# Kernel tuning notes

Measured on AMD Instinct MI355X. Metric: run time of the kernel, lower is better.

## Reference

```python
import jax, jax.numpy as jnp
import numpy as np

DEPTH = 18                      # perfect binary tree depth -> N = 2**DEPTH - 1 nodes
N_NODES = 2 ** DEPTH - 1        # 262143
VOCAB, E, H = 2048, 64, 64


def setup_inputs() -> dict:
    key = jax.random.key(0)
    ks = jax.random.split(key, 10)
    token_ids = jax.random.randint(ks[0], (N_NODES,), 0, VOCAB, dtype=jnp.int32)
    emb = jax.random.normal(ks[1], (VOCAB, E), dtype=jnp.float32)
    emb = emb.at[0].set(0.0)  # padding_idx=0 row is zero in torch
    s = 0.1  # keep gates out of hard saturation
    return {
        "token_ids": token_ids,
        "emb": emb,
        "W_iou": jax.random.normal(ks[2], (3 * H, E), dtype=jnp.float32) * s,
        "b_Wiou": jnp.zeros((3 * H,), dtype=jnp.float32),
        "U_iou": jax.random.normal(ks[3], (3 * H, 2 * H), dtype=jnp.float32) * s,
        "b_Uiou": jnp.zeros((3 * H,), dtype=jnp.float32),
        "W_f": jax.random.normal(ks[4], (2 * H, E), dtype=jnp.float32) * s,
        "b_Wf": jnp.zeros((2 * H,), dtype=jnp.float32),
        "U_f": jax.random.normal(ks[5], (2 * H, 2 * H), dtype=jnp.float32) * s,
        "b_Uf": jnp.zeros((2 * H,), dtype=jnp.float32),
        "depth": DEPTH,
    }


def _tree_lstm(token_ids, emb, W_iou, b_Wiou, U_iou, b_Uiou, W_f, b_Wf, U_f, b_Uf, depth):
    """Level-synchronous bottom-up Binary TreeLSTM over a perfect binary tree.

    Node i has children 2i+1 (left), 2i+2 (right); level l occupies
    indices [2**l - 1, 2**(l+1) - 2]. Children of level-l node k sit at
    offsets 2k, 2k+1 of level l+1, so a reshape gives (left, right) pairs.
    """
    Hd = W_f.shape[0] // 2
    h = c = None
    for l in range(depth - 1, -1, -1):
        start, n = 2 ** l - 1, 2 ** l
        x = emb[token_ids[start:start + n]]                    # [n, E]
        if h is None:  # leaves: zero left/right states (both children zero)
            h_cat = jnp.zeros((n, 2 * Hd), dtype=x.dtype)
            c_lr = jnp.zeros((n, 2, Hd), dtype=x.dtype)
        else:
            h_cat = h.reshape(n, 2 * Hd)                        # [h_l | h_r]
            c_lr = c.reshape(n, 2, Hd)
        iou = jax.nn.sigmoid(x @ W_iou.T + b_Wiou + h_cat @ U_iou.T + b_Uiou)
        i_g, o_g, u_g = jnp.split(iou, 3, axis=1)
        u_g = jnp.tanh(u_g)  # faithful: tanh(sigmoid(u_pre)) as in the source
        f = jax.nn.sigmoid(x @ W_f.T + b_Wf + h_cat @ U_f.T + b_Uf)
        f_l, f_r = f[:, :Hd], f[:, Hd:]
        c = i_g * u_g + f_l * c_lr[:, 0] + f_r * c_lr[:, 1]
        h = o_g * jnp.tanh(c)
    return jnp.stack([h, c])  # [2, 1, H]: root (h, c)


def reference(token_ids, emb, W_iou, b_Wiou, U_iou, b_Uiou, W_f, b_Wf, U_f, b_Uf, depth):
    return _tree_lstm(token_ids, emb, W_iou, b_Wiou, U_iou, b_Uiou,
                      W_f, b_Wf, U_f, b_Uf, depth)
```

## Files before the change

### kernel.cpp

```cpp
#include <hip/hip_runtime.h>

typedef __bf16 bf16;
typedef __bf16 bf16x8 __attribute__((ext_vector_type(8)));
typedef float f32x4 __attribute__((ext_vector_type(4)));

#define DEPTH   18
#define N_NODES ((1 << DEPTH) - 1)
#define KDIM    192
#define RDIM    320
#define A_PAD   200
#define LOG2E   1.4426950408889634f

__device__ __forceinline__ float rcpf(float x) { return __builtin_amdgcn_rcpf(x); }
__device__ __forceinline__ float sig2(float p)  { return rcpf(1.f + exp2f(-p)); }
__device__ __forceinline__ float tanhf_(float x){ return 2.f * rcpf(1.f + exp2f(-2.f * LOG2E * x)) - 1.f; }

__device__ __forceinline__ void gates(const f32x4* acc,
        const float4& bI, const float4& bO, const float4& bU,
        const float4& bL, const float4& bR,
        const float4& cl, const float4& cr, float4& c4, float4& h4) {
    const float* pbI = &bI.x; const float* pbO = &bO.x; const float* pbU = &bU.x;
    const float* pbL = &bL.x; const float* pbR = &bR.x;
    const float* pcl = &cl.x; const float* pcr = &cr.x;
    float* pc4 = &c4.x; float* ph4 = &h4.x;
#pragma unroll
    for (int r = 0; r < 4; r++) {
        float i_g = sig2(acc[0][r] + pbI[r]);
        float o_g = sig2(acc[1][r] + pbO[r]);
        float u_g = tanhf_(sig2(acc[2][r] + pbU[r]));
        float fl  = sig2(acc[3][r] + pbL[r]);
        float fr  = sig2(acc[4][r] + pbR[r]);
        float c = i_g * u_g + fl * pcl[r] + fr * pcr[r];
        pc4[r] = c;
        ph4[r] = o_g * tanhf_(c);
    }
}

__global__ void prep_all(const float* __restrict__ emb,
                     const float* __restrict__ W_iou, const float* __restrict__ U_iou,
                     const float* __restrict__ W_f,   const float* __restrict__ U_f,
                     const float* __restrict__ b_Wiou, const float* __restrict__ b_Uiou,
                     const float* __restrict__ b_Wf,   const float* __restrict__ b_Uf,
                     bf16* __restrict__ Wcat, float* __restrict__ bias, bf16* __restrict__ emb16,
                     bf16* __restrict__ leafH, float* __restrict__ leafC) {
    __shared__ __align__(16) bf16 Wl[192 * 72];
    __shared__ __align__(16) bf16 Al[64 * 72];
    const int blk = blockIdx.x, tid = threadIdx.x;
    if (blk < 512) {
        int t = blk * 256 + tid;
        emb16[t] = (bf16)emb[t];
        if (t < RDIM * KDIM) {
            int r = t / KDIM, k = t % KDIM;
            float v;
            if (r < 192) v = (k < 64) ? W_iou[r * 64 + k] : U_iou[r * 128 + (k - 64)];
            else { int rr = r - 192; v = (k < 64) ? W_f[rr * 64 + k] : U_f[rr * 128 + (k - 64)]; }
            Wcat[t] = (bf16)(v * LOG2E);
        }
        if (t < RDIM)
            bias[t] = ((t < 192) ? (b_Wiou[t] + b_Uiou[t]) : (b_Wf[t - 192] + b_Uf[t - 192])) * LOG2E;
        return;
    }
    const int v0 = (blk - 512) * 64;
    for (int i = tid; i < 192 * 64; i += 256) {
        int r = i >> 6, k = i & 63;
        Wl[r * 72 + k] = (bf16)(W_iou[i] * LOG2E);
    }
    for (int i = tid; i < 64 * 64; i += 256) {
        int r = i >> 6, k = i & 63;
        Al[r * 72 + k] = (bf16)emb[(v0 << 6) + i];
    }
    __syncthreads();
    const int wave = tid >> 6, lane = tid & 63;
    const int l15 = lane & 15, quad = lane >> 4;
    const int jw = (wave & 3) * 16, jb = jw + quad * 4;

    f32x4 acc[4][3];
#pragma unroll
    for (int t = 0; t < 4; t++)
#pragma unroll
        for (int g = 0; g < 3; g++) acc[t][g] = (f32x4){0.f, 0.f, 0.f, 0.f};
#pragma unroll
    for (int kb = 0; kb < 2; kb++) {
        bf16x8 wfrag[3], nfrag[4];
#pragma unroll
        for (int g = 0; g < 3; g++)
            wfrag[g] = *(const bf16x8*)(&Wl[(g * 64 + jw + l15) * 72 + kb * 32 + quad * 8]);
#pragma unroll
        for (int t = 0; t < 4; t++)
            nfrag[t] = *(const bf16x8*)(&Al[(t * 16 + l15) * 72 + kb * 32 + quad * 8]);
#pragma unroll
        for (int t = 0; t < 4; t++)
#pragma unroll
            for (int g = 0; g < 3; g++)
                acc[t][g] = __builtin_amdgcn_mfma_f32_16x16x32_bf16(wfrag[g], nfrag[t], acc[t][g], 0, 0, 0);
    }
    float4 bW, bU_;
    bW = *(const float4*)(b_Wiou + jb);       bU_ = *(const float4*)(b_Uiou + jb);
    float4 bI = make_float4((bW.x + bU_.x) * LOG2E, (bW.y + bU_.y) * LOG2E, (bW.z + bU_.z) * LOG2E, (bW.w + bU_.w) * LOG2E);
    bW = *(const float4*)(b_Wiou + 64 + jb);  bU_ = *(const float4*)(b_Uiou + 64 + jb);
    float4 bO = make_float4((bW.x + bU_.x) * LOG2E, (bW.y + bU_.y) * LOG2E, (bW.z + bU_.z) * LOG2E, (bW.w + bU_.w) * LOG2E);
    bW = *(const float4*)(b_Wiou + 128 + jb); bU_ = *(const float4*)(b_Uiou + 128 + jb);
    float4 bU = make_float4((bW.x + bU_.x) * LOG2E, (bW.y + bU_.y) * LOG2E, (bW.z + bU_.z) * LOG2E, (bW.w + bU_.w) * LOG2E);
    const float* pbI = &bI.x; const float* pbO = &bO.x; const float* pbU = &bU.x;
#pragma unroll
    for (int t = 0; t < 4; t++) {
        int v = v0 + t * 16 + l15;
        float4 c4; float* pc4 = &c4.x;
        union { bf16 h[4]; uint2 u; } hp;
#pragma unroll
        for (int r = 0; r < 4; r++) {
            float i_g = sig2(acc[t][0][r] + pbI[r]);
            float o_g = sig2(acc[t][1][r] + pbO[r]);
            float u_g = tanhf_(sig2(acc[t][2][r] + pbU[r]));
            float c = i_g * u_g;
            pc4[r] = c;
            hp.h[r] = (bf16)(o_g * tanhf_(c));
        }
        *(float4*)(leafC + (size_t)v * 64 + jb) = c4;
        *(uint2*)(leafH + (size_t)v * 64 + jb) = hp.u;
    }
}

template<int NQ, bool CGLOB>
__device__ __forceinline__ void level_phase(
        int l, int blk, int tid, int wt, int l15, int quad, int jb,
        const bf16x8 (&Wf)[5][6],
        const float4& bI, const float4& bO, const float4& bU,
        const float4& bL, const float4& bR,
        bf16* Acur, bf16* Anx,
        const bf16* __restrict__ emb16, const int* __restrict__ token_ids,
        bf16* __restrict__ H, float* __restrict__ c_buf)
{
    const int m = 1 << (l - 8);
    const int s = (1 << l) - 1, o = blk * m;
    const int T = (m + 15) >> 4;
    const int mn = m >> 1;
    const float* Cin = (const float*)(Acur + m * A_PAD);

    float4 pcl[NQ], pcr[NQ];
    int pidx[NQ], pgn[NQ]; bool pact[NQ];
#pragma unroll
    for (int q = 0; q < NQ; q++) {
        int ti = wt + 2 * q;
        int idx0 = ti * 16 + l15;
        bool act = (ti < T) && (idx0 < m);
        int idx = act ? idx0 : 0;
        pidx[q] = idx; pact[q] = act; pgn[q] = s + o + idx;
        if (CGLOB) {
            pcl[q] = *(const float4*)(c_buf + (size_t)(2 * pgn[q] + 1) * 64 + jb);
            pcr[q] = *(const float4*)(c_buf + (size_t)(2 * pgn[q] + 2) * 64 + jb);
        } else {
            pcl[q] = *(const float4*)(Cin + (2 * idx) * 68 + jb);
            pcr[q] = *(const float4*)(Cin + (2 * idx + 1) * 68 + jb);
        }
    }

    int tok = 0;
    const int srow = tid >> 3, sk8 = (tid & 7) << 3;
    const bool sact = (l > 8) && (tid < mn * 8);
    if (sact) tok = token_ids[(1 << (l - 1)) - 1 + blk * mn + srow];

    float* Cout = (float*)(Anx + mn * A_PAD);
#pragma unroll
    for (int q = 0; q < NQ; q++) {
        f32x4 acc[5];
#pragma unroll
        for (int g = 0; g < 5; g++) acc[g] = (f32x4){0.f, 0.f, 0.f, 0.f};
#pragma unroll
        for (int kb = 0; kb < 6; kb++) {
            bf16x8 nf = *(const bf16x8*)(&Acur[pidx[q] * A_PAD + kb * 32 + quad * 8]);
#pragma unroll
            for (int g = 0; g < 5; g++)
                acc[g] = __builtin_amdgcn_mfma_f32_16x16x32_bf16(Wf[g][kb], nf, acc[g], 0, 0, 0);
        }
        float4 c4, h4;
        gates(acc, bI, bO, bU, bL, bR, pcl[q], pcr[q], c4, h4);
        if (pact[q]) {
            union { bf16 h[4]; uint2 u; } hp;
            const float* ph4 = &h4.x;
#pragma unroll
            for (int r = 0; r < 4; r++) hp.h[r] = (bf16)ph4[r];
            if (l > 8) {
                *(float4*)(Cout + pidx[q] * 68 + jb) = c4;
                *(uint2*)(&Anx[(pidx[q] >> 1) * A_PAD + 64 + (pidx[q] & 1) * 64 + jb]) = hp.u;
            } else {
                *(float4*)(c_buf + (size_t)pgn[q] * 64 + jb) = c4;
                *(uint2*)(H + (size_t)pgn[q] * 64 + jb) = hp.u;
            }
        }
    }

    if (sact) {
        uint4 g = *(const uint4*)(emb16 + (size_t)tok * 64 + sk8);
        *(uint4*)(&Anx[srow * A_PAD + sk8]) = g;
    }
    __syncthreads();
}

__global__ __launch_bounds__(512, 1) void big_pass(
        const bf16* __restrict__ Wcat, const float* __restrict__ bias,
        const bf16* __restrict__ emb16, const int* __restrict__ token_ids,
        const bf16* __restrict__ leafH, const float* __restrict__ leafC,
        bf16* __restrict__ H, float* __restrict__ c_buf) {
    __shared__ __align__(16) bf16 A0[256 * A_PAD];
    __shared__ __align__(16) bf16 A1[128 * A_PAD];
    const int tid = threadIdx.x, blk = blockIdx.x;
    const int wave = tid >> 6, lane = tid & 63;
    const int l15 = lane & 15, quad = lane >> 4;
    const int wj = wave & 3, wt = wave >> 2;
    const int jw = wj * 16, jb = jw + quad * 4;

    const int base16 = 65535 + blk * 256;

    for (int ch = tid; ch < 256 * 8; ch += 512) {
        int row = ch >> 3, k8 = (ch & 7) << 3;
        int tok = token_ids[base16 + row];
        *(uint4*)&A0[row * A_PAD + k8] = *(const uint4*)(emb16 + tok * 64 + k8);
    }
    for (int ch = tid; ch < 256 * 16; ch += 512) {
        int row = ch >> 4, half = (ch >> 3) & 1, k8 = (ch & 7) << 3;
        int tok = token_ids[2 * (base16 + row) + 1 + half];
        *(uint4*)&A0[row * A_PAD + 64 + half * 64 + k8] = *(const uint4*)(leafH + (size_t)tok * 64 + k8);
    }

    int tkl16[8], tkr16[8];
#pragma unroll
    for (int q = 0; q < 8; q++) {
        int idx = (wt + 2 * q) * 16 + l15;
        int gn = base16 + idx;
        tkl16[q] = token_ids[2 * gn + 1];
        tkr16[q] = token_ids[2 * gn + 2];
    }
    const int rowa = tid >> 3, k8a = (tid & 7) << 3;
    const int rowb = (tid + 512) >> 3, k8b = k8a;
    const int tok15a = token_ids[32767 + blk * 128 + rowa];
    const int tok15b = token_ids[32767 + blk * 128 + rowb];

    bf16x8 Wf[5][6];
#pragma unroll
    for (int g = 0; g < 5; g++)
#pragma unroll
        for (int kb = 0; kb < 6; kb++)
            Wf[g][kb] = *(const bf16x8*)(Wcat + (g * 64 + jw + l15) * KDIM + kb * 32 + quad * 8);

    const float4 bI = *(const float4*)(bias + jb);
    const float4 bO = *(const float4*)(bias + 64 + jb);
    const float4 bU = *(const float4*)(bias + 128 + jb);
    const float4 bL = *(const float4*)(bias + 192 + jb);
    const float4 bR = *(const float4*)(bias + 256 + jb);
    __syncthreads();

#pragma unroll
    for (int grp = 0; grp < 2; grp++) {
        float4 cl4[4], cr4[4];
#pragma unroll
        for (int q = 0; q < 4; q++) {
            cl4[q] = *(const float4*)(leafC + (size_t)tkl16[grp * 4 + q] * 64 + jb);
            cr4[q] = *(const float4*)(leafC + (size_t)tkr16[grp * 4 + q] * 64 + jb);
        }
#pragma unroll
        for (int q = 0; q < 4; q++) {
            const int idx = (wt + 2 * (grp * 4 + q)) * 16 + l15;
            const int gn = base16 + idx;
            f32x4 acc[5];
#pragma unroll
            for (int g = 0; g < 5; g++) acc[g] = (f32x4){0.f, 0.f, 0.f, 0.f};
#pragma unroll
            for (int kb = 0; kb < 6; kb++) {
                bf16x8 nf = *(const bf16x8*)(&A0[idx * A_PAD + kb * 32 + quad * 8]);
#pragma unroll
                for (int g = 0; g < 5; g++)
                    acc[g] = __builtin_amdgcn_mfma_f32_16x16x32_bf16(Wf[g][kb], nf, acc[g], 0, 0, 0);
            }
            float4 c4, h4;
            gates(acc, bI, bO, bU, bL, bR, cl4[q], cr4[q], c4, h4);
            union { bf16 h[4]; uint2 u; } hp;
            const float* ph4 = &h4.x;
#pragma unroll
            for (int r = 0; r < 4; r++) hp.h[r] = (bf16)ph4[r];
            *(float4*)(c_buf + (size_t)gn * 64 + jb) = c4;
            *(uint2*)(&A1[(idx >> 1) * A_PAD + 64 + (idx & 1) * 64 + jb]) = hp.u;
        }
        if (grp == 0) {
            uint4 ga = *(const uint4*)(emb16 + (size_t)tok15a * 64 + k8a);
            uint4 gb = *(const uint4*)(emb16 + (size_t)tok15b * 64 + k8b);
            *(uint4*)(&A1[rowa * A_PAD + k8a]) = ga;
            *(uint4*)(&A1[rowb * A_PAD + k8b]) = gb;
        }
    }
    __syncthreads();

    bf16* Acur = A1;
    bf16* Anx  = A0;
    level_phase<4, true >(15, blk, tid, wt, l15, quad, jb, Wf, bI, bO, bU, bL, bR,
                          Acur, Anx, emb16, token_ids, H, c_buf);
    { bf16* t = Acur; Acur = Anx; Anx = t; }
    level_phase<2, false>(14, blk, tid, wt, l15, quad, jb, Wf, bI, bO, bU, bL, bR,
                          Acur, Anx, emb16, token_ids, H, c_buf);
    { bf16* t = Acur; Acur = Anx; Anx = t; }
    for (int l = 13; l >= 8; l--) {
        level_phase<1, false>(l, blk, tid, wt, l15, quad, jb, Wf, bI, bO, bU, bL, bR,
                              Acur, Anx, emb16, token_ids, H, c_buf);
        bf16* t = Acur; Acur = Anx; Anx = t;
    }
}

__global__ __launch_bounds__(512) void tail_pass(
        const bf16* __restrict__ Wcat, const float* __restrict__ bias,
        const bf16* __restrict__ emb16, const int* __restrict__ token_ids,
        const bf16* __restrict__ H, const float* __restrict__ c_buf,
        float* __restrict__ out) {
    __shared__ __align__(16) bf16 A[255 * A_PAD];
    __shared__ __align__(16) float C0[128 * 68];
    __shared__ __align__(16) float C1[64 * 68];
    const int tid = threadIdx.x;
    const int wave = tid >> 6, lane = tid & 63;
    const int l15 = lane & 15, quad = lane >> 4;
    const int wj = wave & 3, wt = wave >> 2;
    const int jw = wj * 16, jb = jw + quad * 4;

    float4 cl7[4], cr7[4];
#pragma unroll
    for (int q = 0; q < 4; q++) {
        int idx = (wt + 2 * q) * 16 + l15;
        int gn = 127 + idx;
        cl7[q] = *(const float4*)(c_buf + (size_t)(2 * gn + 1) * 64 + jb);
        cr7[q] = *(const float4*)(c_buf + (size_t)(2 * gn + 2) * 64 + jb);
    }

    for (int ch = tid; ch < 255 * 8; ch += 512) {
        int row = ch >> 3, k8 = (ch & 7) << 3;
        int l = 31 - __clz(255 - row);
        int idx = row - 256 + (2 << l);
        int gn = (1 << l) - 1 + idx;
        int tok = token_ids[gn];
        *(uint4*)&A[row * A_PAD + k8] = *(const uint4*)(emb16 + tok * 64 + k8);
    }
    for (int ch = tid; ch < 128 * 16; ch += 512) {
        int row = ch >> 4, k8 = (ch & 15) << 3;
        *(uint4*)&A[row * A_PAD + 64 + k8] =
            *(const uint4*)(H + (size_t)(255 + 2 * row) * 64 + k8);
    }

    bf16x8 Wf[5][6];
#pragma unroll
    for (int g = 0; g < 5; g++)
#pragma unroll
        for (int kb = 0; kb < 6; kb++)
            Wf[g][kb] = *(const bf16x8*)(Wcat + (g * 64 + jw + l15) * KDIM + kb * 32 + quad * 8);

    const float4 bI = *(const float4*)(bias + jb);
    const float4 bO = *(const float4*)(bias + 64 + jb);
    const float4 bU = *(const float4*)(bias + 128 + jb);
    const float4 bL = *(const float4*)(bias + 192 + jb);
    const float4 bR = *(const float4*)(bias + 256 + jb);
    __syncthreads();

#pragma unroll
    for (int q = 0; q < 4; q++) {
        const int idx = (wt + 2 * q) * 16 + l15;
        f32x4 acc[5];
#pragma unroll
        for (int g = 0; g < 5; g++) acc[g] = (f32x4){0.f, 0.f, 0.f, 0.f};
#pragma unroll
        for (int kb = 0; kb < 6; kb++) {
            bf16x8 nf = *(const bf16x8*)(&A[idx * A_PAD + kb * 32 + quad * 8]);
#pragma unroll
            for (int g = 0; g < 5; g++)
                acc[g] = __builtin_amdgcn_mfma_f32_16x16x32_bf16(Wf[g][kb], nf, acc[g], 0, 0, 0);
        }
        float4 c4, h4;
        gates(acc, bI, bO, bU, bL, bR, cl7[q], cr7[q], c4, h4);
        union { bf16 h[4]; uint2 u; } hp;
        const float* ph4 = &h4.x;
#pragma unroll
        for (int r = 0; r < 4; r++) hp.h[r] = (bf16)ph4[r];
        *(float4*)(C0 + idx * 68 + jb) = c4;
        *(uint2*)(&A[(128 + (idx >> 1)) * A_PAD + 64 + (idx & 1) * 64 + jb]) = hp.u;
    }
    __syncthreads();

    float* Ccur = C0;
    float* Cnx  = C1;
    for (int l = 6; l >= 0; l--) {
        const int n = 1 << l;
        const int off  = 256 - 2 * n;
        const int offn = 256 - n;
        const int T = (n + 15) >> 4;
        for (int ti = wt; ti < T; ti += 2) {
            int idx0 = ti * 16 + l15;
            int idx = idx0 < n ? idx0 : n - 1;
            float4 cl = *(const float4*)(Ccur + (2 * idx) * 68 + jb);
            float4 cr = *(const float4*)(Ccur + (2 * idx + 1) * 68 + jb);
            f32x4 acc[5];
#pragma unroll
            for (int g = 0; g < 5; g++) acc[g] = (f32x4){0.f, 0.f, 0.f, 0.f};
#pragma unroll
            for (int kb = 0; kb < 6; kb++) {
                bf16x8 nf = *(const bf16x8*)(&A[(off + idx) * A_PAD + kb * 32 + quad * 8]);
#pragma unroll
                for (int g = 0; g < 5; g++)
                    acc[g] = __builtin_amdgcn_mfma_f32_16x16x32_bf16(Wf[g][kb], nf, acc[g], 0, 0, 0);
            }
            float4 c4, h4;
            gates(acc, bI, bO, bU, bL, bR, cl, cr, c4, h4);
            if (idx0 < n) {
                if (l > 0) {
                    union { bf16 h[4]; uint2 u; } hp;
                    const float* ph4 = &h4.x;
#pragma unroll
                    for (int r = 0; r < 4; r++) hp.h[r] = (bf16)ph4[r];
                    *(float4*)(Cnx + idx * 68 + jb) = c4;
                    *(uint2*)(&A[(offn + (idx >> 1)) * A_PAD + 64 + (idx & 1) * 64 + jb]) = hp.u;
                } else {
                    *(float4*)(out + jb) = h4;
                    *(float4*)(out + 64 + jb) = c4;
                }
            }
        }
        __syncthreads();
        float* t = Ccur; Ccur = Cnx; Cnx = t;
    }
}

extern "C" void kernel_launch(void* const* d_in, const int* in_sizes, int n_in,
                              void* d_out, int out_size, void* d_ws, size_t ws_size,
                              hipStream_t stream) {
    const int*   token_ids = (const int*)d_in[0];
    const float* emb       = (const float*)d_in[1];
    const float* W_iou     = (const float*)d_in[2];
    const float* b_Wiou    = (const float*)d_in[3];
    const float* U_iou     = (const float*)d_in[4];
    const float* b_Uiou    = (const float*)d_in[5];
    const float* W_f       = (const float*)d_in[6];
    const float* b_Wf      = (const float*)d_in[7];
    const float* U_f       = (const float*)d_in[8];
    const float* b_Uf      = (const float*)d_in[9];
    float* out = (float*)d_out;

    char* ws = (char*)d_ws;
    bf16*  Wcat  = (bf16*)ws;
    float* bias  = (float*)(ws + 122880);
    bf16*  emb16 = (bf16*)(ws + 124160);
    bf16*  leafH = (bf16*)(ws + 386304);
    float* leafC = (float*)(ws + 648448);
    bf16*  H     = (bf16*)(ws + 1172736);
    float* c_buf = (float*)(ws + 1238272);

    prep_all<<<544, 256, 0, stream>>>(emb, W_iou, U_iou, W_f, U_f,
                                      b_Wiou, b_Uiou, b_Wf, b_Uf,
                                      Wcat, bias, emb16, leafH, leafC);
    big_pass<<<256, 512, 0, stream>>>(Wcat, bias, emb16, token_ids, leafH, leafC, H, c_buf);
    tail_pass<<<1, 512, 0, stream>>>(Wcat, bias, emb16, token_ids, H, c_buf, out);
}
```

Baseline: 162.1 us.

## Fuse prep, big pass and tail into one cooperative kernel with grid syncs

Merges the three separate kernel launches (weight/embedding prep plus leaf computation, the per-block subtree pass, and the single-block tail) into one cooperative kernel. Grid-wide barriers replace the kernel boundaries. The leaf precompute is redistributed over the first 32 blocks of 512 threads, and shared memory is unified into one buffer reused by each phase. This removes launch gaps and kernel-boundary drains. In exchange it adds cooperative-launch overhead and grid-sync cost, and 255 blocks sit idle while block 0 runs the tail.

Result: slower. 236.0 us (+45.6%).

```diff
diff --git a/kernel.cpp b/kernel.cpp
--- a/kernel.cpp
+++ b/kernel.cpp
@@ -1,4 +1,7 @@
 #include <hip/hip_runtime.h>
+#include <hip/hip_cooperative_groups.h>
+
+namespace cg = cooperative_groups;
 
 typedef __bf16 bf16;
 typedef __bf16 bf16x8 __attribute__((ext_vector_type(8)));
@@ -33,91 +36,6 @@
         float c = i_g * u_g + fl * pcl[r] + fr * pcr[r];
         pc4[r] = c;
         ph4[r] = o_g * tanhf_(c);
-    }
-}
-
-__global__ void prep_all(const float* __restrict__ emb,
-                     const float* __restrict__ W_iou, const float* __restrict__ U_iou,
-                     const float* __restrict__ W_f,   const float* __restrict__ U_f,
-                     const float* __restrict__ b_Wiou, const float* __restrict__ b_Uiou,
-                     const float* __restrict__ b_Wf,   const float* __restrict__ b_Uf,
-                     bf16* __restrict__ Wcat, float* __restrict__ bias, bf16* __restrict__ emb16,
-                     bf16* __restrict__ leafH, float* __restrict__ leafC) {
-    __shared__ __align__(16) bf16 Wl[192 * 72];
-    __shared__ __align__(16) bf16 Al[64 * 72];
-    const int blk = blockIdx.x, tid = threadIdx.x;
-    if (blk < 512) {
-        int t = blk * 256 + tid;
-        emb16[t] = (bf16)emb[t];
-        if (t < RDIM * KDIM) {
-            int r = t / KDIM, k = t % KDIM;
-            float v;
-            if (r < 192) v = (k < 64) ? W_iou[r * 64 + k] : U_iou[r * 128 + (k - 64)];
-            else { int rr = r - 192; v = (k < 64) ? W_f[rr * 64 + k] : U_f[rr * 128 + (k - 64)]; }
-            Wcat[t] = (bf16)(v * LOG2E);
-        }
-        if (t < RDIM)
-            bias[t] = ((t < 192) ? (b_Wiou[t] + b_Uiou[t]) : (b_Wf[t - 192] + b_Uf[t - 192])) * LOG2E;
-        return;
-    }
-    const int v0 = (blk - 512) * 64;
-    for (int i = tid; i < 192 * 64; i += 256) {
-        int r = i >> 6, k = i & 63;
-        Wl[r * 72 + k] = (bf16)(W_iou[i] * LOG2E);
-    }
-    for (int i = tid; i < 64 * 64; i += 256) {
-        int r = i >> 6, k = i & 63;
-        Al[r * 72 + k] = (bf16)emb[(v0 << 6) + i];
-    }
-    __syncthreads();
-    const int wave = tid >> 6, lane = tid & 63;
-    const int l15 = lane & 15, quad = lane >> 4;
-    const int jw = (wave & 3) * 16, jb = jw + quad * 4;
-
-    f32x4 acc[4][3];
-#pragma unroll
-    for (int t = 0; t < 4; t++)
-#pragma unroll
-        for (int g = 0; g < 3; g++) acc[t][g] = (f32x4){0.f, 0.f, 0.f, 0.f};
-#pragma unroll
-    for (int kb = 0; kb < 2; kb++) {
-        bf16x8 wfrag[3], nfrag[4];
-#pragma unroll
-        for (int g = 0; g < 3; g++)
-            wfrag[g] = *(const bf16x8*)(&Wl[(g * 64 + jw + l15) * 72 + kb * 32 + quad * 8]);
-#pragma unroll
-        for (int t = 0; t < 4; t++)
-            nfrag[t] = *(const bf16x8*)(&Al[(t * 16 + l15) * 72 + kb * 32 + quad * 8]);
-#pragma unroll
-        for (int t = 0; t < 4; t++)
-#pragma unroll
-            for (int g = 0; g < 3; g++)
-                acc[t][g] = __builtin_amdgcn_mfma_f32_16x16x32_bf16(wfrag[g], nfrag[t], acc[t][g], 0, 0, 0);
-    }
-    float4 bW, bU_;
-    bW = *(const float4*)(b_Wiou + jb);       bU_ = *(const float4*)(b_Uiou + jb);
-    float4 bI = make_float4((bW.x + bU_.x) * LOG2E, (bW.y + bU_.y) * LOG2E, (bW.z + bU_.z) * LOG2E, (bW.w + bU_.w) * LOG2E);
-    bW = *(const float4*)(b_Wiou + 64 + jb);  bU_ = *(const float4*)(b_Uiou + 64 + jb);
-    float4 bO = make_float4((bW.x + bU_.x) * LOG2E, (bW.y + bU_.y) * LOG2E, (bW.z + bU_.z) * LOG2E, (bW.w + bU_.w) * LOG2E);
-    bW = *(const float4*)(b_Wiou + 128 + jb); bU_ = *(const float4*)(b_Uiou + 128 + jb);
-    float4 bU = make_float4((bW.x + bU_.x) * LOG2E, (bW.y + bU_.y) * LOG2E, (bW.z + bU_.z) * LOG2E, (bW.w + bU_.w) * LOG2E);
-    const float* pbI = &bI.x; const float* pbO = &bO.x; const float* pbU = &bU.x;
-#pragma unroll
-    for (int t = 0; t < 4; t++) {
-        int v = v0 + t * 16 + l15;
-        float4 c4; float* pc4 = &c4.x;
-        union { bf16 h[4]; uint2 u; } hp;
-#pragma unroll
-        for (int r = 0; r < 4; r++) {
-            float i_g = sig2(acc[t][0][r] + pbI[r]);
-            float o_g = sig2(acc[t][1][r] + pbO[r]);
-            float u_g = tanhf_(sig2(acc[t][2][r] + pbU[r]));
-            float c = i_g * u_g;
-            pc4[r] = c;
-            hp.h[r] = (bf16)(o_g * tanhf_(c));
-        }
-        *(float4*)(leafC + (size_t)v * 64 + jb) = c4;
-        *(uint2*)(leafH + (size_t)v * 64 + jb) = hp.u;
     }
 }
 
@@ -197,229 +115,306 @@
     __syncthreads();
 }
 
-__global__ __launch_bounds__(512, 1) void big_pass(
-        const bf16* __restrict__ Wcat, const float* __restrict__ bias,
-        const bf16* __restrict__ emb16, const int* __restrict__ token_ids,
-        const bf16* __restrict__ leafH, const float* __restrict__ leafC,
-        bf16* __restrict__ H, float* __restrict__ c_buf) {
-    __shared__ __align__(16) bf16 A0[256 * A_PAD];
-    __shared__ __align__(16) bf16 A1[128 * A_PAD];
+__global__ __launch_bounds__(512, 1) void fused_all(
+        const float* __restrict__ emb,
+        const float* __restrict__ W_iou, const float* __restrict__ U_iou,
+        const float* __restrict__ W_f,   const float* __restrict__ U_f,
+        const float* __restrict__ b_Wiou, const float* __restrict__ b_Uiou,
+        const float* __restrict__ b_Wf,   const float* __restrict__ b_Uf,
+        const int* __restrict__ token_ids,
+        bf16* __restrict__ Wcat, float* __restrict__ bias, bf16* __restrict__ emb16,
+        bf16* __restrict__ leafH, float* __restrict__ leafC,
+        bf16* __restrict__ H, float* __restrict__ c_buf, float* __restrict__ out)
+{
+    __shared__ __align__(16) char smem[154224];
     const int tid = threadIdx.x, blk = blockIdx.x;
     const int wave = tid >> 6, lane = tid & 63;
     const int l15 = lane & 15, quad = lane >> 4;
     const int wj = wave & 3, wt = wave >> 2;
     const int jw = wj * 16, jb = jw + quad * 4;
 
-    const int base16 = 65535 + blk * 256;
-
-    for (int ch = tid; ch < 256 * 8; ch += 512) {
-        int row = ch >> 3, k8 = (ch & 7) << 3;
-        int tok = token_ids[base16 + row];
-        *(uint4*)&A0[row * A_PAD + k8] = *(const uint4*)(emb16 + tok * 64 + k8);
-    }
-    for (int ch = tid; ch < 256 * 16; ch += 512) {
-        int row = ch >> 4, half = (ch >> 3) & 1, k8 = (ch & 7) << 3;
-        int tok = token_ids[2 * (base16 + row) + 1 + half];
-        *(uint4*)&A0[row * A_PAD + 64 + half * 64 + k8] = *(const uint4*)(leafH + (size_t)tok * 64 + k8);
-    }
-
-    int tkl16[8], tkr16[8];
-#pragma unroll
-    for (int q = 0; q < 8; q++) {
-        int idx = (wt + 2 * q) * 16 + l15;
-        int gn = base16 + idx;
-        tkl16[q] = token_ids[2 * gn + 1];
-        tkr16[q] = token_ids[2 * gn + 2];
-    }
-    const int rowa = tid >> 3, k8a = (tid & 7) << 3;
-    const int rowb = (tid + 512) >> 3, k8b = k8a;
-    const int tok15a = token_ids[32767 + blk * 128 + rowa];
-    const int tok15b = token_ids[32767 + blk * 128 + rowb];
-
-    bf16x8 Wf[5][6];
-#pragma unroll
-    for (int g = 0; g < 5; g++)
-#pragma unroll
-        for (int kb = 0; kb < 6; kb++)
-            Wf[g][kb] = *(const bf16x8*)(Wcat + (g * 64 + jw + l15) * KDIM + kb * 32 + quad * 8);
-
-    const float4 bI = *(const float4*)(bias + jb);
-    const float4 bO = *(const float4*)(bias + 64 + jb);
-    const float4 bU = *(const float4*)(bias + 128 + jb);
-    const float4 bL = *(const float4*)(bias + 192 + jb);
-    const float4 bR = *(const float4*)(bias + 256 + jb);
-    __syncthreads();
-
-#pragma unroll
-    for (int grp = 0; grp < 2; grp++) {
-        float4 cl4[4], cr4[4];
+    {
+        int t = blk * 512 + tid;
+        emb16[t] = (bf16)emb[t];
+        if (t < RDIM * KDIM) {
+            int r = t / KDIM, k = t % KDIM;
+            float v;
+            if (r < 192) v = (k < 64) ? W_iou[r * 64 + k] : U_iou[r * 128 + (k - 64)];
+            else { int rr = r - 192; v = (k < 64) ? W_f[rr * 64 + k] : U_f[rr * 128 + (k - 64)]; }
+            Wcat[t] = (bf16)(v * LOG2E);
+        }
+        if (t < RDIM)
+            bias[t] = ((t < 192) ? (b_Wiou[t] + b_Uiou[t]) : (b_Wf[t - 192] + b_Uf[t - 192])) * LOG2E;
+    }
+    if (blk < 32) {
+        bf16* Wl = (bf16*)smem;
+        bf16* Al = (bf16*)(smem + 27648);
+        const int v0 = blk * 64;
+        for (int i = tid; i < 192 * 64; i += 512) {
+            int r = i >> 6, k = i & 63;
+            Wl[r * 72 + k] = (bf16)(W_iou[i] * LOG2E);
+        }
+        for (int i = tid; i < 64 * 64; i += 512) {
+            int r = i >> 6, k = i & 63;
+            Al[r * 72 + k] = (bf16)emb[(v0 << 6) + i];
+        }
+        __syncthreads();
+
+        f32x4 acc[2][3];
+#pragma unroll
+        for (int t = 0; t < 2; t++)
+#pragma unroll
+            for (int g = 0; g < 3; g++) acc[t][g] = (f32x4){0.f, 0.f, 0.f, 0.f};
+#pragma unroll
+        for (int kb = 0; kb < 2; kb++) {
+            bf16x8 wfrag[3], nfrag[2];
+#pragma unroll
+            for (int g = 0; g < 3; g++)
+                wfrag[g] = *(const bf16x8*)(&Wl[(g * 64 + jw + l15) * 72 + kb * 32 + quad * 8]);
+#pragma unroll
+            for (int t = 0; t < 2; t++)
+                nfrag[t] = *(const bf16x8*)(&Al[((wt * 2 + t) * 16 + l15) * 72 + kb * 32 + quad * 8]);
+#pragma unroll
+            for (int t = 0; t < 2; t++)
+#pragma unroll
+                for (int g = 0; g < 3; g++)
+                    acc[t][g] = __builtin_amdgcn_mfma_f32_16x16x32_bf16(wfrag[g], nfrag[t], acc[t][g], 0, 0, 0);
+        }
+        float4 bW, bU_;
+        bW = *(const float4*)(b_Wiou + jb);       bU_ = *(const float4*)(b_Uiou + jb);
+        float4 bI = make_float4((bW.x + bU_.x) * LOG2E, (bW.y + bU_.y) * LOG2E, (bW.z + bU_.z) * LOG2E, (bW.w + bU_.w) * LOG2E);
+        bW = *(const float4*)(b_Wiou + 64 + jb);  bU_ = *(const float4*)(b_Uiou + 64 + jb);
+        float4 bO = make_float4((bW.x + bU_.x) * LOG2E, (bW.y + bU_.y) * LOG2E, (bW.z + bU_.z) * LOG2E, (bW.w + bU_.w) * LOG2E);
+        bW = *(const float4*)(b_Wiou + 128 + jb); bU_ = *(const float4*)(b_Uiou + 128 + jb);
+        float4 bU = make_float4((bW.x + bU_.x) * LOG2E, (bW.y + bU_.y) * LOG2E, (bW.z + bU_.z) * LOG2E, (bW.w + bU_.w) * LOG2E);
+        const float* pbI = &bI.x; const float* pbO = &bO.x; const float* pbU = &bU.x;
+#pragma unroll
+        for (int t = 0; t < 2; t++) {
+            int v = v0 + (wt * 2 + t) * 16 + l15;
+            float4 c4; float* pc4 = &c4.x;
+            union { bf16 h[4]; uint2 u; } hp;
+#pragma unroll
+            for (int r = 0; r < 4; r++) {
+                float i_g = sig2(acc[t][0][r] + pbI[r]);
+                float o_g = sig2(acc[t][1][r] + pbO[r]);
+                float u_g = tanhf_(sig2(acc[t][2][r] + pbU[r]));
+                float c = i_g * u_g;
+                pc4[r] = c;
+                hp.h[r] = (bf16)(o_g * tanhf_(c));
+            }
+            *(float4*)(leafC + (size_t)v * 64 + jb) = c4;
+            *(uint2*)(leafH + (size_t)v * 64 + jb) = hp.u;
+        }
+    }
+    cg::this_grid().sync();
+
+    {
+        bf16* A0 = (bf16*)smem;
+        bf16* A1 = (bf16*)(smem + 102400);
+        const int base16 = 65535 + blk * 256;
+
+        for (int ch = tid; ch < 256 * 8; ch += 512) {
+            int row = ch >> 3, k8 = (ch & 7) << 3;
+            int tok = token_ids[base16 + row];
+            *(uint4*)&A0[row * A_PAD + k8] = *(const uint4*)(emb16 + tok * 64 + k8);
+        }
+        for (int ch = tid; ch < 256 * 16; ch += 512) {
+            int row = ch >> 4, half = (ch >> 3) & 1, k8 = (ch & 7) << 3;
+            int tok = token_ids[2 * (base16 + row) + 1 + half];
+            *(uint4*)&A0[row * A_PAD + 64 + half * 64 + k8] = *(const uint4*)(leafH + (size_t)tok * 64 + k8);
+        }
+
+        int tkl16[8], tkr16[8];
+#pragma unroll
+        for (int q = 0; q < 8; q++) {
+            int idx = (wt + 2 * q) * 16 + l15;
+            int gn = base16 + idx;
+            tkl16[q] = token_ids[2 * gn + 1];
+            tkr16[q] = token_ids[2 * gn + 2];
+        }
+        const int rowa = tid >> 3, k8a = (tid & 7) << 3;
+        const int rowb = (tid + 512) >> 3, k8b = k8a;
+        const int tok15a = token_ids[32767 + blk * 128 + rowa];
+        const int tok15b = token_ids[32767 + blk * 128 + rowb];
+
+        bf16x8 Wf[5][6];
+#pragma unroll
+        for (int g = 0; g < 5; g++)
+#pragma unroll
+            for (int kb = 0; kb < 6; kb++)
+                Wf[g][kb] = *(const bf16x8*)(Wcat + (g * 64 + jw + l15) * KDIM + kb * 32 + quad * 8);
+
+        const float4 bI = *(const float4*)(bias + jb);
+        const float4 bO = *(const float4*)(bias + 64 + jb);
+        const float4 bU = *(const float4*)(bias + 128 + jb);
+        const float4 bL = *(const float4*)(bias + 192 + jb);
+        const float4 bR = *(const float4*)(bias + 256 + jb);
+        __syncthreads();
+
+#pragma unroll
+        for (int grp = 0; grp < 2; grp++) {
+            float4 cl4[4], cr4[4];
+#pragma unroll
+            for (int q = 0; q < 4; q++) {
+                cl4[q] = *(const float4*)(leafC + (size_t)tkl16[grp * 4 + q] * 64 + jb);
+                cr4[q] = *(const float4*)(leafC + (size_t)tkr16[grp * 4 + q] * 64 + jb);
+            }
+#pragma unroll
+            for (int q = 0; q < 4; q++) {
+                const int idx = (wt + 2 * (grp * 4 + q)) * 16 + l15;
+                const int gn = base16 + idx;
+                f32x4 acc[5];
+#pragma unroll
+                for (int g = 0; g < 5; g++) acc[g] = (f32x4){0.f, 0.f, 0.f, 0.f};
+#pragma unroll
+                for (int kb = 0; kb < 6; kb++) {
+                    bf16x8 nf = *(const bf16x8*)(&A0[idx * A_PAD + kb * 32 + quad * 8]);
+#pragma unroll
+                    for (int g = 0; g < 5; g++)
+                        acc[g] = __builtin_amdgcn_mfma_f32_16x16x32_bf16(Wf[g][kb], nf, acc[g], 0, 0, 0);
+                }
+                float4 c4, h4;
+                gates(acc, bI, bO, bU, bL, bR, cl4[q], cr4[q], c4, h4);
+                union { bf16 h[4]; uint2 u; } hp;
+                const float* ph4 = &h4.x;
+#pragma unroll
+                for (int r = 0; r < 4; r++) hp.h[r] = (bf16)ph4[r];
+                *(float4*)(c_buf + (size_t)gn * 64 + jb) = c4;
+                *(uint2*)(&A1[(idx >> 1) * A_PAD + 64 + (idx & 1) * 64 + jb]) = hp.u;
+            }
+            if (grp == 0) {
+                uint4 ga = *(const uint4*)(emb16 + (size_t)tok15a * 64 + k8a);
+                uint4 gb = *(const uint4*)(emb16 + (size_t)tok15b * 64 + k8b);
+                *(uint4*)(&A1[rowa * A_PAD + k8a]) = ga;
+                *(uint4*)(&A1[rowb * A_PAD + k8b]) = gb;
+            }
+        }
+        __syncthreads();
+
+        bf16* Acur = A1;
+        bf16* Anx  = A0;
+        level_phase<4, true >(15, blk, tid, wt, l15, quad, jb, Wf, bI, bO, bU, bL, bR,
+                              Acur, Anx, emb16, token_ids, H, c_buf);
+        { bf16* t = Acur; Acur = Anx; Anx = t; }
+        level_phase<2, false>(14, blk, tid, wt, l15, quad, jb, Wf, bI, bO, bU, bL, bR,
+                              Acur, Anx, emb16, token_ids, H, c_buf);
+        { bf16* t = Acur; Acur = Anx; Anx = t; }
+        for (int l = 13; l >= 8; l--) {
+            level_phase<1, false>(l, blk, tid, wt, l15, quad, jb, Wf, bI, bO, bU, bL, bR,
+                                  Acur, Anx, emb16, token_ids, H, c_buf);
+            bf16* t = Acur; Acur = Anx; Anx = t;
+        }
+    }
+    cg::this_grid().sync();
+
+    if (blk != 0) return;
+    {
+        bf16*  A  = (bf16*)smem;
+        float* C0 = (float*)(smem + 102000);
+        float* C1 = (float*)(smem + 136816);
+
+        float4 cl7[4], cr7[4];
 #pragma unroll
         for (int q = 0; q < 4; q++) {
-            cl4[q] = *(const float4*)(leafC + (size_t)tkl16[grp * 4 + q] * 64 + jb);
-            cr4[q] = *(const float4*)(leafC + (size_t)tkr16[grp * 4 + q] * 64 + jb);
-        }
+            int idx = (wt + 2 * q) * 16 + l15;
+            int gn = 127 + idx;
+            cl7[q] = *(const float4*)(c_buf + (size_t)(2 * gn + 1) * 64 + jb);
+            cr7[q] = *(const float4*)(c_buf + (size_t)(2 * gn + 2) * 64 + jb);
+        }
+
+        for (int ch = tid; ch < 255 * 8; ch += 512) {
+            int row = ch >> 3, k8 = (ch & 7) << 3;
+            int l = 31 - __clz(255 - row);
+            int idx = row - 256 + (2 << l);
+            int gn = (1 << l) - 1 + idx;
+            int tok = token_ids[gn];
+            *(uint4*)&A[row * A_PAD + k8] = *(const uint4*)(emb16 + tok * 64 + k8);
+        }
+        for (int ch = tid; ch < 128 * 16; ch += 512) {
+            int row = ch >> 4, k8 = (ch & 15) << 3;
+            *(uint4*)&A[row * A_PAD + 64 + k8] =
+                *(const uint4*)(H + (size_t)(255 + 2 * row) * 64 + k8);
+        }
+
+        bf16x8 Wf[5][6];
+#pragma unroll
+        for (int g = 0; g < 5; g++)
+#pragma unroll
+            for (int kb = 0; kb < 6; kb++)
+                Wf[g][kb] = *(const bf16x8*)(Wcat + (g * 64 + jw + l15) * KDIM + kb * 32 + quad * 8);
+
+        const float4 bI = *(const float4*)(bias + jb);
+        const float4 bO = *(const float4*)(bias + 64 + jb);
+        const float4 bU = *(const float4*)(bias + 128 + jb);
+        const float4 bL = *(const float4*)(bias + 192 + jb);
+        const float4 bR = *(const float4*)(bias + 256 + jb);
+        __syncthreads();
+
 #pragma unroll
         for (int q = 0; q < 4; q++) {
-            const int idx = (wt + 2 * (grp * 4 + q)) * 16 + l15;
-            const int gn = base16 + idx;
+            const int idx = (wt + 2 * q) * 16 + l15;
             f32x4 acc[5];
 #pragma unroll
             for (int g = 0; g < 5; g++) acc[g] = (f32x4){0.f, 0.f, 0.f, 0.f};
 #pragma unroll
             for (int kb = 0; kb < 6; kb++) {
-                bf16x8 nf = *(const bf16x8*)(&A0[idx * A_PAD + kb * 32 + quad * 8]);
+                bf16x8 nf = *(const bf16x8*)(&A[idx * A_PAD + kb * 32 + quad * 8]);
 #pragma unroll
                 for (int g = 0; g < 5; g++)
                     acc[g] = __builtin_amdgcn_mfma_f32_16x16x32_bf16(Wf[g][kb], nf, acc[g], 0, 0, 0);
             }
             float4 c4, h4;
-            gates(acc, bI, bO, bU, bL, bR, cl4[q], cr4[q], c4, h4);
+            gates(acc, bI, bO, bU, bL, bR, cl7[q], cr7[q], c4, h4);
             union { bf16 h[4]; uint2 u; } hp;
             const float* ph4 = &h4.x;
 #pragma unroll
             for (int r = 0; r < 4; r++) hp.h[r] = (bf16)ph4[r];
-            *(float4*)(c_buf + (size_t)gn * 64 + jb) = c4;
-            *(uint2*)(&A1[(idx >> 1) * A_PAD + 64 + (idx & 1) * 64 + jb]) = hp.u;
-        }
-        if (grp == 0) {
-            uint4 ga = *(const uint4*)(emb16 + (size_t)tok15a * 64 + k8a);
-            uint4 gb = *(const uint4*)(emb16 + (size_t)tok15b * 64 + k8b);
-            *(uint4*)(&A1[rowa * A_PAD + k8a]) = ga;
-            *(uint4*)(&A1[rowb * A_PAD + k8b]) = gb;
-        }
-    }
-    __syncthreads();
-
-    bf16* Acur = A1;
-    bf16* Anx  = A0;
-    level_phase<4, true >(15, blk, tid, wt, l15, quad, jb, Wf, bI, bO, bU, bL, bR,
-                          Acur, Anx, emb16, token_ids, H, c_buf);
-    { bf16* t = Acur; Acur = Anx; Anx = t; }
-    level_phase<2, false>(14, blk, tid, wt, l15, quad, jb, Wf, bI, bO, bU, bL, bR,
-                          Acur, Anx, emb16, token_ids, H, c_buf);
-    { bf16* t = Acur; Acur = Anx; Anx = t; }
-    for (int l = 13; l >= 8; l--) {
-        level_phase<1, false>(l, blk, tid, wt, l15, quad, jb, Wf, bI, bO, bU, bL, bR,
-                              Acur, Anx, emb16, token_ids, H, c_buf);
-        bf16* t = Acur; Acur = Anx; Anx = t;
-    }
-}
-
-__global__ __launch_bounds__(512) void tail_pass(
-        const bf16* __restrict__ Wcat, const float* __restrict__ bias,
-        const bf16* __restrict__ emb16, const int* __restrict__ token_ids,
-        const bf16* __restrict__ H, const float* __restrict__ c_buf,
-        float* __restrict__ out) {
-    __shared__ __align__(16) bf16 A[255 * A_PAD];
-    __shared__ __align__(16) float C0[128 * 68];
-    __shared__ __align__(16) float C1[64 * 68];
-    const int tid = threadIdx.x;
-    const int wave = tid >> 6, lane = tid & 63;
-    const int l15 = lane & 15, quad = lane >> 4;
-    const int wj = wave & 3, wt = wave >> 2;
-    const int jw = wj * 16, jb = jw + quad * 4;
-
-    float4 cl7[4], cr7[4];
-#pragma unroll
-    for (int q = 0; q < 4; q++) {
-        int idx = (wt + 2 * q) * 16 + l15;
-        int gn = 127 + idx;
-        cl7[q] = *(const float4*)(c_buf + (size_t)(2 * gn + 1) * 64 + jb);
-        cr7[q] = *(const float4*)(c_buf + (size_t)(2 * gn + 2) * 64 + jb);
-    }
-
-    for (int ch = tid; ch < 255 * 8; ch += 512) {
-        int row = ch >> 3, k8 = (ch & 7) << 3;
-        int l = 31 - __clz(255 - row);
-        int idx = row - 256 + (2 << l);
-        int gn = (1 << l) - 1 + idx;
-        int tok = token_ids[gn];
-        *(uint4*)&A[row * A_PAD + k8] = *(const uint4*)(emb16 + tok * 64 + k8);
-    }
-    for (int ch = tid; ch < 128 * 16; ch += 512) {
-        int row = ch >> 4, k8 = (ch & 15) << 3;
-        *(uint4*)&A[row * A_PAD + 64 + k8] =
-            *(const uint4*)(H + (size_t)(255 + 2 * row) * 64 + k8);
-    }
-
-    bf16x8 Wf[5][6];
-#pragma unroll
-    for (int g = 0; g < 5; g++)
-#pragma unroll
-        for (int kb = 0; kb < 6; kb++)
-            Wf[g][kb] = *(const bf16x8*)(Wcat + (g * 64 + jw + l15) * KDIM + kb * 32 + quad * 8);
-
-    const float4 bI = *(const float4*)(bias + jb);
-    const float4 bO = *(const float4*)(bias + 64 + jb);
-    const float4 bU = *(const float4*)(bias + 128 + jb);
-    const float4 bL = *(const float4*)(bias + 192 + jb);
-    const float4 bR = *(const float4*)(bias + 256 + jb);
-    __syncthreads();
-
-#pragma unroll
-    for (int q = 0; q < 4; q++) {
-        const int idx = (wt + 2 * q) * 16 + l15;
-        f32x4 acc[5];
-#pragma unroll
-        for (int g = 0; g < 5; g++) acc[g] = (f32x4){0.f, 0.f, 0.f, 0.f};
-#pragma unroll
-        for (int kb = 0; kb < 6; kb++) {
-            bf16x8 nf = *(const bf16x8*)(&A[idx * A_PAD + kb * 32 + quad * 8]);
-#pragma unroll
-            for (int g = 0; g < 5; g++)
-                acc[g] = __builtin_amdgcn_mfma_f32_16x16x32_bf16(Wf[g][kb], nf, acc[g], 0, 0, 0);
-        }
-        float4 c4, h4;
-        gates(acc, bI, bO, bU, bL, bR, cl7[q], cr7[q], c4, h4);
-        union { bf16 h[4]; uint2 u; } hp;
-        const float* ph4 = &h4.x;
-#pragma unroll
-        for (int r = 0; r < 4; r++) hp.h[r] = (bf16)ph4[r];
-        *(float4*)(C0 + idx * 68 + jb) = c4;
-        *(uint2*)(&A[(128 + (idx >> 1)) * A_PAD + 64 + (idx & 1) * 64 + jb]) = hp.u;
-    }
-    __syncthreads();
-
-    float* Ccur = C0;
-    float* Cnx  = C1;
-    for (int l = 6; l >= 0; l--) {
-        const int n = 1 << l;
-        const int off  = 256 - 2 * n;
-        const int offn = 256 - n;
-        const int T = (n + 15) >> 4;
-        for (int ti = wt; ti < T; ti += 2) {
-            int idx0 = ti * 16 + l15;
-            int idx = idx0 < n ? idx0 : n - 1;
-            float4 cl = *(const float4*)(Ccur + (2 * idx) * 68 + jb);
-            float4 cr = *(const float4*)(Ccur + (2 * idx + 1) * 68 + jb);
-            f32x4 acc[5];
-#pragma unroll
-            for (int g = 0; g < 5; g++) acc[g] = (f32x4){0.f, 0.f, 0.f, 0.f};
-#pragma unroll
-            for (int kb = 0; kb < 6; kb++) {
-                bf16x8 nf = *(const bf16x8*)(&A[(off + idx) * A_PAD + kb * 32 + quad * 8]);
-#pragma unroll
-                for (int g = 0; g < 5; g++)
-                    acc[g] = __builtin_amdgcn_mfma_f32_16x16x32_bf16(Wf[g][kb], nf, acc[g], 0, 0, 0);
-            }
-            float4 c4, h4;
-            gates(acc, bI, bO, bU, bL, bR, cl, cr, c4, h4);
-            if (idx0 < n) {
-                if (l > 0) {
-                    union { bf16 h[4]; uint2 u; } hp;
-                    const float* ph4 = &h4.x;
-#pragma unroll
-                    for (int r = 0; r < 4; r++) hp.h[r] = (bf16)ph4[r];
-                    *(float4*)(Cnx + idx * 68 + jb) = c4;
-                    *(uint2*)(&A[(offn + (idx >> 1)) * A_PAD + 64 + (idx & 1) * 64 + jb]) = hp.u;
-                } else {
-                    *(float4*)(out + jb) = h4;
-                    *(float4*)(out + 64 + jb) = c4;
+            *(float4*)(C0 + idx * 68 + jb) = c4;
+            *(uint2*)(&A[(128 + (idx >> 1)) * A_PAD + 64 + (idx & 1) * 64 + jb]) = hp.u;
+        }
+        __syncthreads();
+
+        float* Ccur = C0;
+        float* Cnx  = C1;
+        for (int l = 6; l >= 0; l--) {
+            const int n = 1 << l;
+            const int off  = 256 - 2 * n;
+            const int offn = 256 - n;
+            const int T = (n + 15) >> 4;
+            for (int ti = wt; ti < T; ti += 2) {
+                int idx0 = ti * 16 + l15;
+                int idx = idx0 < n ? idx0 : n - 1;
+                float4 cl = *(const float4*)(Ccur + (2 * idx) * 68 + jb);
+                float4 cr = *(const float4*)(Ccur + (2 * idx + 1) * 68 + jb);
+                f32x4 acc[5];
+#pragma unroll
+                for (int g = 0; g < 5; g++) acc[g] = (f32x4){0.f, 0.f, 0.f, 0.f};
+#pragma unroll
+                for (int kb = 0; kb < 6; kb++) {
+                    bf16x8 nf = *(const bf16x8*)(&A[(off + idx) * A_PAD + kb * 32 + quad * 8]);
+#pragma unroll
+                    for (int g = 0; g < 5; g++)
+                        acc[g] = __builtin_amdgcn_mfma_f32_16x16x32_bf16(Wf[g][kb], nf, acc[g], 0, 0, 0);
                 }
-            }
-        }
-        __syncthreads();
-        float* t = Ccur; Ccur = Cnx; Cnx = t;
+                float4 c4, h4;
+                gates(acc, bI, bO, bU, bL, bR, cl, cr, c4, h4);
+                if (idx0 < n) {
+                    if (l > 0) {
+                        union { bf16 h[4]; uint2 u; } hp;
+                        const float* ph4 = &h4.x;
+#pragma unroll
+                        for (int r = 0; r < 4; r++) hp.h[r] = (bf16)ph4[r];
+                        *(float4*)(Cnx + idx * 68 + jb) = c4;
+                        *(uint2*)(&A[(offn + (idx >> 1)) * A_PAD + 64 + (idx & 1) * 64 + jb]) = hp.u;
+                    } else {
+                        *(float4*)(out + jb) = h4;
+                        *(float4*)(out + 64 + jb) = c4;
+                    }
+                }
+            }
+            __syncthreads();
+            float* t = Ccur; Ccur = Cnx; Cnx = t;
+        }
     }
 }
 
@@ -447,9 +442,13 @@
     bf16*  H     = (bf16*)(ws + 1172736);
     float* c_buf = (float*)(ws + 1238272);
 
-    prep_all<<<544, 256, 0, stream>>>(emb, W_iou, U_iou, W_f, U_f,
-                                      b_Wiou, b_Uiou, b_Wf, b_Uf,
-                                      Wcat, bias, emb16, leafH, leafC);
-    big_pass<<<256, 512, 0, stream>>>(Wcat, bias, emb16, token_ids, leafH, leafC, H, c_buf);
-    tail_pass<<<1, 512, 0, stream>>>(Wcat, bias, emb16, token_ids, H, c_buf, out);
+    void* args[] = {
+        (void*)&emb, (void*)&W_iou, (void*)&U_iou, (void*)&W_f, (void*)&U_f,
+        (void*)&b_Wiou, (void*)&b_Uiou, (void*)&b_Wf, (void*)&b_Uf,
+        (void*)&token_ids,
+        (void*)&Wcat, (void*)&bias, (void*)&emb16, (void*)&leafH, (void*)&leafC,
+        (void*)&H, (void*)&c_buf, (void*)&out
+    };
+    hipLaunchCooperativeKernel((const void*)fused_all, dim3(256), dim3(512),
+                               args, 0, stream);
 }
```

## Split levels 16 and 15 into separate wide-grid kernels before mid pass

Applied to the files above, without the earlier changes.

Levels 16 and 15 move out of the 256-block fused kernel into standalone per-level kernels launched with 512 and 256 blocks. These kernels pass h and c through global memory instead of shared memory. The fused kernel now starts at level 14, uses less LDS, and reads level-15 outputs from global H. The aim is more parallelism and occupancy on the widest levels, at the cost of extra launches and global round-trips. The H and c_buf workspace layout is widened so node-indexed storage fits for all levels.

After: 188.9 us. +16.6%, slower.

```diff
diff --git a/kernel.cpp b/kernel.cpp
--- a/kernel.cpp
+++ b/kernel.cpp
@@ -121,6 +121,94 @@
     }
 }
 
+template<bool LEAF>
+__global__ __launch_bounds__(512, 1) void par_level(
+        const bf16* __restrict__ Wcat, const float* __restrict__ bias,
+        const bf16* __restrict__ emb16, const int* __restrict__ token_ids,
+        const bf16* __restrict__ leafH, const float* __restrict__ leafC,
+        bf16* __restrict__ H, float* __restrict__ c_buf, int s) {
+    __shared__ __align__(16) bf16 A[128 * A_PAD];
+    const int tid = threadIdx.x, blk = blockIdx.x;
+    const int wave = tid >> 6, lane = tid & 63;
+    const int l15 = lane & 15, quad = lane >> 4;
+    const int wj = wave & 3, wt = wave >> 2;
+    const int jw = wj * 16, jb = jw + quad * 4;
+    const int base = s + blk * 128;
+
+    for (int ch = tid; ch < 128 * 8; ch += 512) {
+        int row = ch >> 3, k8 = (ch & 7) << 3;
+        int tok = token_ids[base + row];
+        *(uint4*)&A[row * A_PAD + k8] = *(const uint4*)(emb16 + tok * 64 + k8);
+    }
+    for (int ch = tid; ch < 128 * 16; ch += 512) {
+        int row = ch >> 4, half = (ch >> 3) & 1, k8 = (ch & 7) << 3;
+        if (LEAF) {
+            int tok = token_ids[2 * (base + row) + 1 + half];
+            *(uint4*)&A[row * A_PAD + 64 + half * 64 + k8] = *(const uint4*)(leafH + (size_t)tok * 64 + k8);
+        } else {
+            *(uint4*)&A[row * A_PAD + 64 + half * 64 + k8] =
+                *(const uint4*)(H + (size_t)(2 * (base + row) + 1 + half) * 64 + k8);
+        }
+    }
+
+    int tkl[4], tkr[4];
+    if (LEAF) {
+#pragma unroll
+        for (int q = 0; q < 4; q++) {
+            int idx = (wt + 2 * q) * 16 + l15;
+            int gn = base + idx;
+            tkl[q] = token_ids[2 * gn + 1];
+            tkr[q] = token_ids[2 * gn + 2];
+        }
+    }
+
+    bf16x8 Wf[5][6];
+#pragma unroll
+    for (int g = 0; g < 5; g++)
+#pragma unroll
+        for (int kb = 0; kb < 6; kb++)
+            Wf[g][kb] = *(const bf16x8*)(Wcat + (g * 64 + jw + l15) * KDIM + kb * 32 + quad * 8);
+
+    const float4 bI = *(const float4*)(bias + jb);
+    const float4 bO = *(const float4*)(bias + 64 + jb);
+    const float4 bU = *(const float4*)(bias + 128 + jb);
+    const float4 bL = *(const float4*)(bias + 192 + jb);
+    const float4 bR = *(const float4*)(bias + 256 + jb);
+    __syncthreads();
+
+#pragma unroll
+    for (int q = 0; q < 4; q++) {
+        const int idx = (wt + 2 * q) * 16 + l15;
+        const int gn = base + idx;
+        float4 cl, cr;
+        if (LEAF) {
+            cl = *(const float4*)(leafC + (size_t)tkl[q] * 64 + jb);
+            cr = *(const float4*)(leafC + (size_t)tkr[q] * 64 + jb);
+        } else {
+            cl = *(const float4*)(c_buf + (size_t)(2 * gn + 1) * 64 + jb);
+            cr = *(const float4*)(c_buf + (size_t)(2 * gn + 2) * 64 + jb);
+        }
+        f32x4 acc[5];
+#pragma unroll
+        for (int g = 0; g < 5; g++) acc[g] = (f32x4){0.f, 0.f, 0.f, 0.f};
+#pragma unroll
+        for (int kb = 0; kb < 6; kb++) {
+            bf16x8 nf = *(const bf16x8*)(&A[idx * A_PAD + kb * 32 + quad * 8]);
+#pragma unroll
+            for (int g = 0; g < 5; g++)
+                acc[g] = __builtin_amdgcn_mfma_f32_16x16x32_bf16(Wf[g][kb], nf, acc[g], 0, 0, 0);
+        }
+        float4 c4, h4;
+        gates(acc, bI, bO, bU, bL, bR, cl, cr, c4, h4);
+        union { bf16 h[4]; uint2 u; } hp;
+        const float* ph4 = &h4.x;
+#pragma unroll
+        for (int r = 0; r < 4; r++) hp.h[r] = (bf16)ph4[r];
+        *(float4*)(c_buf + (size_t)gn * 64 + jb) = c4;
+        *(uint2*)(H + (size_t)gn * 64 + jb) = hp.u;
+    }
+}
+
 template<int NQ, bool CGLOB>
 __device__ __forceinline__ void level_phase(
         int l, int blk, int tid, int wt, int l15, int quad, int jb,
@@ -197,44 +285,28 @@
     __syncthreads();
 }
 
-__global__ __launch_bounds__(512, 1) void big_pass(
+__global__ __launch_bounds__(512, 1) void mid_pass(
         const bf16* __restrict__ Wcat, const float* __restrict__ bias,
         const bf16* __restrict__ emb16, const int* __restrict__ token_ids,
-        const bf16* __restrict__ leafH, const float* __restrict__ leafC,
         bf16* __restrict__ H, float* __restrict__ c_buf) {
-    __shared__ __align__(16) bf16 A0[256 * A_PAD];
-    __shared__ __align__(16) bf16 A1[128 * A_PAD];
+    __shared__ __align__(16) bf16 A0[64 * A_PAD];
+    __shared__ __align__(16) bf16 A1[80 * A_PAD];
     const int tid = threadIdx.x, blk = blockIdx.x;
     const int wave = tid >> 6, lane = tid & 63;
     const int l15 = lane & 15, quad = lane >> 4;
     const int wj = wave & 3, wt = wave >> 2;
     const int jw = wj * 16, jb = jw + quad * 4;
 
-    const int base16 = 65535 + blk * 256;
-
-    for (int ch = tid; ch < 256 * 8; ch += 512) {
-        int row = ch >> 3, k8 = (ch & 7) << 3;
-        int tok = token_ids[base16 + row];
+    {
+        int row = tid >> 3, k8 = (tid & 7) << 3;
+        int tok = token_ids[16383 + blk * 64 + row];
         *(uint4*)&A0[row * A_PAD + k8] = *(const uint4*)(emb16 + tok * 64 + k8);
     }
-    for (int ch = tid; ch < 256 * 16; ch += 512) {
+    for (int ch = tid; ch < 64 * 16; ch += 512) {
         int row = ch >> 4, half = (ch >> 3) & 1, k8 = (ch & 7) << 3;
-        int tok = token_ids[2 * (base16 + row) + 1 + half];
-        *(uint4*)&A0[row * A_PAD + 64 + half * 64 + k8] = *(const uint4*)(leafH + (size_t)tok * 64 + k8);
-    }
-
-    int tkl16[8], tkr16[8];
-#pragma unroll
-    for (int q = 0; q < 8; q++) {
-        int idx = (wt + 2 * q) * 16 + l15;
-        int gn = base16 + idx;
-        tkl16[q] = token_ids[2 * gn + 1];
-        tkr16[q] = token_ids[2 * gn + 2];
-    }
-    const int rowa = tid >> 3, k8a = (tid & 7) << 3;
-    const int rowb = (tid + 512) >> 3, k8b = k8a;
-    const int tok15a = token_ids[32767 + blk * 128 + rowa];
-    const int tok15b = token_ids[32767 + blk * 128 + rowb];
+        *(uint4*)&A0[row * A_PAD + 64 + half * 64 + k8] =
+            *(const uint4*)(H + (size_t)(2 * (16383 + blk * 64 + row) + 1 + half) * 64 + k8);
+    }
 
     bf16x8 Wf[5][6];
 #pragma unroll
@@ -250,52 +322,9 @@
     const float4 bR = *(const float4*)(bias + 256 + jb);
     __syncthreads();
 
-#pragma unroll
-    for (int grp = 0; grp < 2; grp++) {
-        float4 cl4[4], cr4[4];
-#pragma unroll
-        for (int q = 0; q < 4; q++) {
-            cl4[q] = *(const float4*)(leafC + (size_t)tkl16[grp * 4 + q] * 64 + jb);
-            cr4[q] = *(const float4*)(leafC + (size_t)tkr16[grp * 4 + q] * 64 + jb);
-        }
-#pragma unroll
-        for (int q = 0; q < 4; q++) {
-            const int idx = (wt + 2 * (grp * 4 + q)) * 16 + l15;
-            const int gn = base16 + idx;
-            f32x4 acc[5];
-#pragma unroll
-            for (int g = 0; g < 5; g++) acc[g] = (f32x4){0.f, 0.f, 0.f, 0.f};
-#pragma unroll
-            for (int kb = 0; kb < 6; kb++) {
-                bf16x8 nf = *(const bf16x8*)(&A0[idx * A_PAD + kb * 32 + quad * 8]);
-#pragma unroll
-                for (int g = 0; g < 5; g++)
-                    acc[g] = __builtin_amdgcn_mfma_f32_16x16x32_bf16(Wf[g][kb], nf, acc[g], 0, 0, 0);
-            }
-            float4 c4, h4;
-            gates(acc, bI, bO, bU, bL, bR, cl4[q], cr4[q], c4, h4);
-            union { bf16 h[4]; uint2 u; } hp;
-            const float* ph4 = &h4.x;
-#pragma unroll
-            for (int r = 0; r < 4; r++) hp.h[r] = (bf16)ph4[r];
-            *(float4*)(c_buf + (size_t)gn * 64 + jb) = c4;
-            *(uint2*)(&A1[(idx >> 1) * A_PAD + 64 + (idx & 1) * 64 + jb]) = hp.u;
-        }
-        if (grp == 0) {
-            uint4 ga = *(const uint4*)(emb16 + (size_t)tok15a * 64 + k8a);
-            uint4 gb = *(const uint4*)(emb16 + (size_t)tok15b * 64 + k8b);
-            *(uint4*)(&A1[rowa * A_PAD + k8a]) = ga;
-            *(uint4*)(&A1[rowb * A_PAD + k8b]) = gb;
-        }
-    }
-    __syncthreads();
-
-    bf16* Acur = A1;
-    bf16* Anx  = A0;
-    level_phase<4, true >(15, blk, tid, wt, l15, quad, jb, Wf, bI, bO, bU, bL, bR,
-                          Acur, Anx, emb16, token_ids, H, c_buf);
-    { bf16* t = Acur; Acur = Anx; Anx = t; }
-    level_phase<2, false>(14, blk, tid, wt, l15, quad, jb, Wf, bI, bO, bU, bL, bR,
+    bf16* Acur = A0;
+    bf16* Anx  = A1;
+    level_phase<2, true >(14, blk, tid, wt, l15, quad, jb, Wf, bI, bO, bU, bL, bR,
                           Acur, Anx, emb16, token_ids, H, c_buf);
     { bf16* t = Acur; Acur = Anx; Anx = t; }
     for (int l = 13; l >= 8; l--) {
@@ -445,11 +474,15 @@
     bf16*  leafH = (bf16*)(ws + 386304);
     float* leafC = (float*)(ws + 648448);
     bf16*  H     = (bf16*)(ws + 1172736);
-    float* c_buf = (float*)(ws + 1238272);
+    float* c_buf = (float*)(ws + 17949952);
 
     prep_all<<<544, 256, 0, stream>>>(emb, W_iou, U_iou, W_f, U_f,
                                       b_Wiou, b_Uiou, b_Wf, b_Uf,
                                       Wcat, bias, emb16, leafH, leafC);
-    big_pass<<<256, 512, 0, stream>>>(Wcat, bias, emb16, token_ids, leafH, leafC, H, c_buf);
+    par_level<true ><<<512, 512, 0, stream>>>(Wcat, bias, emb16, token_ids,
+                                              leafH, leafC, H, c_buf, 65535);
+    par_level<false><<<256, 512, 0, stream>>>(Wcat, bias, emb16, token_ids,
+                                              leafH, leafC, H, c_buf, 32767);
+    mid_pass<<<256, 512, 0, stream>>>(Wcat, bias, emb16, token_ids, H, c_buf);
     tail_pass<<<1, 512, 0, stream>>>(Wcat, bias, emb16, token_ids, H, c_buf, out);
 }
```
